# Kernel tuning notes

Measured on AMD Instinct MI355X. Metric: run time of the kernel, lower is better.

The kernel has to match this reference:

```python
import jax, jax.numpy as jnp
import numpy as np

D_MODEL = 768
N_HEAD = 12
D_HEAD = D_MODEL // N_HEAD
B, T = 2, 2048


def setup_inputs() -> dict:
    key = jax.random.key(0)
    k1, k2, k3 = jax.random.split(key, 3)
    x = jax.random.normal(k1, (B, T, D_MODEL), dtype=jnp.float32)
    w_attn = jax.random.normal(k2, (D_MODEL, 3 * D_MODEL), dtype=jnp.float32) * (1.0 / np.sqrt(D_MODEL))
    b_attn = jnp.zeros((3 * D_MODEL,), dtype=jnp.float32)
    w_proj = jax.random.normal(k3, (D_MODEL, D_MODEL), dtype=jnp.float32) * (1.0 / np.sqrt(D_MODEL))
    b_proj = jnp.zeros((D_MODEL,), dtype=jnp.float32)
    return {"x": x, "w_attn": w_attn, "b_attn": b_attn, "w_proj": w_proj, "b_proj": b_proj}


def reference(x, w_attn, b_attn, w_proj, b_proj):
    Bq, Tq, C = x.shape
    qkv = x @ w_attn + b_attn                                  # [B, T, 3C]
    qkv = qkv.reshape(Bq, Tq, 3, N_HEAD, D_HEAD)
    q, k, v = qkv[:, :, 0], qkv[:, :, 1], qkv[:, :, 2]         # [B, T, H, Dh]
    scale = 1.0 / np.sqrt(D_HEAD)
    att = jnp.einsum('bqhd,bkhd->bhqk', q, k) * scale          # [B, H, T, T]
    causal = jnp.tril(jnp.ones((Tq, Tq), dtype=bool))
    att = jnp.where(causal[None, None], att, -jnp.inf)
    att = jax.nn.softmax(att, axis=-1)
    y = jnp.einsum('bhqk,bkhd->bqhd', att, v).reshape(Bq, Tq, C)
    return y @ w_proj + b_proj
```

## Files before the change

kernel.cpp:

```cpp
#include <hip/hip_runtime.h>
#include <hip/hip_bf16.h>

#define D_MODEL 768
#define N_HEADS 12
#define D_HEADK 64
#define BB 2
#define TT 2048
#define M_TOK (BB*TT)
#define N_QKV (3*D_MODEL)
#define MS_SEG (BB*N_HEADS*TT)

using f32x4  = __attribute__((ext_vector_type(4))) float;
using f32x16 = __attribute__((ext_vector_type(16))) float;
using s16x8  = __attribute__((ext_vector_type(8))) short;

__device__ __forceinline__ float fast_exp2(float x) {
    return __builtin_amdgcn_exp2f(x);
}

__device__ __forceinline__ unsigned short f2bf(float f) {
    union { float f; unsigned u; } v; v.f = f;
    unsigned r = v.u + 0x7FFFu + ((v.u >> 16) & 1u);
    return (unsigned short)(r >> 16);
}

__device__ __forceinline__ float bf2f(unsigned short u) {
    union { unsigned u; float f; } v; v.u = ((unsigned)u) << 16; return v.f;
}

__device__ __forceinline__ unsigned cvtpk_bf16(float lo, float hi) {
    unsigned d;
    asm("v_cvt_pk_bf16_f32 %0, %1, %2" : "=v"(d) : "v"(lo), "v"(hi));
    return d;
}

__global__ void xbf_kernel(const float* __restrict__ X, unsigned short* __restrict__ Xb) {
    int idx = (blockIdx.x * 256 + threadIdx.x) * 8;
    float4 v0 = *(const float4*)&X[idx];
    float4 v1 = *(const float4*)&X[idx + 4];
    ushort4 u0, u1;
    u0.x = f2bf(v0.x); u0.y = f2bf(v0.y); u0.z = f2bf(v0.z); u0.w = f2bf(v0.w);
    u1.x = f2bf(v1.x); u1.y = f2bf(v1.y); u1.z = f2bf(v1.z); u1.w = f2bf(v1.w);
    *(ushort4*)&Xb[idx]     = u0;
    *(ushort4*)&Xb[idx + 4] = u1;
}

__global__ void wtrans_kernel(const float* __restrict__ Wa, const float* __restrict__ Wp,
                              unsigned short* __restrict__ Wta, unsigned short* __restrict__ Wtp) {
    const float* W; unsigned short* Wt; int N;
    if (blockIdx.z == 0) { W = Wa; Wt = Wta; N = N_QKV; }
    else                 { W = Wp; Wt = Wtp; N = D_MODEL; }
    int bx = blockIdx.x * 32;
    if (bx >= N) return;
    int by = blockIdx.y * 32;
    __shared__ float tile[32][33];
    int tx = threadIdx.x & 31;
    int ty = threadIdx.x >> 5;
    #pragma unroll
    for (int i = ty; i < 32; i += 8)
        tile[i][tx] = W[(size_t)(by + i) * N + bx + tx];
    __syncthreads();
    #pragma unroll
    for (int i = ty; i < 32; i += 8)
        Wt[(size_t)(bx + i) * D_MODEL + by + tx] = f2bf(tile[tx][i]);
}

__launch_bounds__(256)
__global__ void qkv_kernel(const unsigned short* __restrict__ Xb, const unsigned short* __restrict__ Wt,
                           const float* __restrict__ bias,
                           unsigned short* __restrict__ Qw, unsigned short* __restrict__ Kw,
                           unsigned short* __restrict__ Vw) {
    __shared__ unsigned short As[128][40];
    __shared__ unsigned short Bs[128][40];
    const int m0 = blockIdx.y * 128;
    const int n0 = blockIdx.x * 128;
    const int tid = threadIdx.x;
    const int l  = tid & 63;
    const int w  = tid >> 6;
    const int wr = w >> 1, wc = w & 1;
    const int lr = l & 15, lk = (l >> 4) * 8, li = (l >> 4) * 4;

    f32x4 acc[4][4] = {};
    for (int kt = 0; kt < D_MODEL; kt += 32) {
        #pragma unroll
        for (int p = 0; p < 2; ++p) {
            int ch = tid * 2 + p;
            int r = ch >> 2;
            int c = (ch & 3) * 8;
            *(int4*)&As[r][c] = *(const int4*)&Xb[(size_t)(m0 + r) * D_MODEL + kt + c];
            *(int4*)&Bs[r][c] = *(const int4*)&Wt[(size_t)(n0 + r) * D_MODEL + kt + c];
        }
        __syncthreads();
        s16x8 a[4], bf[4];
        #pragma unroll
        for (int mi = 0; mi < 4; ++mi)
            a[mi] = *(const s16x8*)&As[wr*64 + mi*16 + lr][lk];
        #pragma unroll
        for (int ni = 0; ni < 4; ++ni)
            bf[ni] = *(const s16x8*)&Bs[wc*64 + ni*16 + lr][lk];
        #pragma unroll
        for (int mi = 0; mi < 4; ++mi)
            #pragma unroll
            for (int ni = 0; ni < 4; ++ni)
                acc[mi][ni] = __builtin_amdgcn_mfma_f32_16x16x32_bf16(a[mi], bf[ni], acc[mi][ni], 0, 0, 0);
        __syncthreads();
    }
    #pragma unroll
    for (int ni = 0; ni < 4; ++ni) {
        int ng = n0 + wc*64 + ni*16 + lr;
        int mat = ng / D_MODEL;
        int hd  = ng % D_MODEL;
        int h = hd >> 6, d = hd & 63;
        float bv = bias[ng];
        #pragma unroll
        for (int mi = 0; mi < 4; ++mi) {
            #pragma unroll
            for (int i = 0; i < 4; ++i) {
                int t  = m0 + wr*64 + mi*16 + li + i;
                int b  = t >> 11, tq = t & 2047;
                float val = acc[mi][ni][i] + bv;
                size_t off = ((size_t)(b*N_HEADS + h)*TT + tq)*64 + d;
                if (mat == 0)      Qw[off] = f2bf(val * 0.18033688f);
                else if (mat == 1) Kw[off] = f2bf(val);
                else               Vw[off] = f2bf(val);
            }
        }
    }
}

__launch_bounds__(256)
__global__ void vtrans_kernel(const unsigned short* __restrict__ Vw, unsigned short* __restrict__ Vt) {
    __shared__ unsigned short tile[64][65];
    const int bh = blockIdx.y;
    const int t0 = blockIdx.x * 64;
    const int tid = threadIdx.x;
    const int srow = tid >> 3;
    const int scol = (tid & 7) * 8;
    const unsigned short* src = Vw + (size_t)bh * TT * 64;
    unsigned short* dst = Vt + (size_t)bh * 64 * TT;
    *(int4*)&tile[srow][scol]    = *(const int4*)&src[(size_t)(t0 + srow) * 64 + scol];
    *(int4*)&tile[srow+32][scol] = *(const int4*)&src[(size_t)(t0 + srow + 32) * 64 + scol];
    __syncthreads();
    s16x8 a0, a1;
    #pragma unroll
    for (int j = 0; j < 8; ++j) {
        a0[j] = (short)tile[scol + j][srow];
        a1[j] = (short)tile[scol + j][srow + 32];
    }
    *(s16x8*)&dst[(size_t)srow * TT + t0 + scol]        = a0;
    *(s16x8*)&dst[(size_t)(srow + 32) * TT + t0 + scol] = a1;
}

__device__ __forceinline__ int swz(int r, int c) { return r*64 + (c ^ ((r & 7) << 3)); }

__launch_bounds__(256)
__global__ void attn_kernel(const unsigned short* __restrict__ Q,
                            const unsigned short* __restrict__ Kk,
                            const unsigned short* __restrict__ Vt,
                            unsigned short* __restrict__ oA,
                            unsigned short* __restrict__ oB,
                            float* __restrict__ ms) {
    __shared__ unsigned short Ks[64*64];
    __shared__ unsigned short Vs[64*64];
    const int bh = blockIdx.y;
    const int px = blockIdx.x;
    const int qci = 15 - (px >> 1);
    const int seg = px & 1;
    const int q0 = qci * 128;
    const int b = bh / N_HEADS, h = bh % N_HEADS;
    const int tid = threadIdx.x;
    const int l  = tid & 63;
    const int w  = tid >> 6;
    const int lq = l & 31;
    const int hi = l >> 5;
    const int srow = tid >> 3;
    const int scol = (tid & 7) * 8;
    const int qw0 = q0 + w * 32;

    const unsigned short* Qp = Q  + (size_t)bh * TT * 64;
    const unsigned short* Kp = Kk + (size_t)bh * TT * 64;
    const unsigned short* Vp = Vt + (size_t)bh * 64 * TT;

    const int ntiles  = 2 * (qci + 1);
    const int n0      = ntiles >> 1;
    const int t_begin = seg ? n0 : 0;
    const int t_end   = seg ? ntiles : n0;

    s16x8 qsel[4];
    {
        const unsigned short* qrow = &Qp[(size_t)(qw0 + lq) * 64];
        #pragma unroll
        for (int t = 0; t < 4; ++t) {
            s16x8 qlo = *(const s16x8*)&qrow[16*t];
            s16x8 qhi = *(const s16x8*)&qrow[16*t + 8];
            qsel[t] = hi ? qhi : qlo;
        }
    }

    float mi = -1e30f, si = 0.f;
    f32x16 o0 = {}, o1 = {};

    const int kb0 = t_begin * 64;
    int4 kp0 = *(const int4*)&Kp[(size_t)(kb0 + srow) * 64 + scol];
    int4 kp1 = *(const int4*)&Kp[(size_t)(kb0 + srow + 32) * 64 + scol];
    int4 vp0 = *(const int4*)&Vp[(size_t)srow * TT + kb0 + scol];
    int4 vp1 = *(const int4*)&Vp[(size_t)(srow + 32) * TT + kb0 + scol];

    for (int it = t_begin; it < t_end; ++it) {
        const int kt = it * 64;
        __syncthreads();
        *(int4*)&Ks[swz(srow,      scol)] = kp0;
        *(int4*)&Ks[swz(srow + 32, scol)] = kp1;
        *(int4*)&Vs[swz(srow,      scol)] = vp0;
        *(int4*)&Vs[swz(srow + 32, scol)] = vp1;
        __syncthreads();
        if (it + 1 < t_end) {
            const int k2 = kt + 64;
            kp0 = *(const int4*)&Kp[(size_t)(k2 + srow) * 64 + scol];
            kp1 = *(const int4*)&Kp[(size_t)(k2 + srow + 32) * 64 + scol];
            vp0 = *(const int4*)&Vp[(size_t)srow * TT + k2 + scol];
            vp1 = *(const int4*)&Vp[(size_t)(srow + 32) * TT + k2 + scol];
        }
        #pragma unroll
        for (int kti = 0; kti < 2; ++kti) {
            const int kk = kt + kti * 32;
            if (kk > qw0) continue;
            const bool diag = (kk == qw0);
            f32x16 s = {};
            #pragma unroll
            for (int t = 0; t < 4; ++t) {
                s16x8 a = *(const s16x8*)&Ks[swz(kti*32 + lq, 16*t + 8*hi)];
                s = __builtin_amdgcn_mfma_f32_32x32x16_bf16(a, qsel[t], s, 0, 0, 0);
            }
            if (diag) {
                #pragma unroll
                for (int r = 0; r < 16; ++r) {
                    const int kloc = (r & 3) + 8*(r >> 2) + 4*hi;
                    if (kloc > lq) s[r] = -1e30f;
                }
            }
            float lm = s[0];
            #pragma unroll
            for (int r = 1; r < 16; ++r) lm = fmaxf(lm, s[r]);
            if (!__all(lm <= mi + 11.5f)) {
                float pm = fmaxf(lm, __shfl_xor(lm, 32));
                float mn = fmaxf(mi, pm);
                float sf = fast_exp2(mi - mn);
                si *= sf;
                #pragma unroll
                for (int r = 0; r < 16; ++r) {
                    const int qloc = (r & 3) + 8*(r >> 2) + 4*hi;
                    float sfq = __shfl(sf, qloc);
                    o0[r] *= sfq; o1[r] *= sfq;
                }
                mi = mn;
            }
            float e[16];
            float psum = 0.f;
            #pragma unroll
            for (int r = 0; r < 16; ++r) {
                e[r] = fast_exp2(s[r] - mi);
                psum += e[r];
            }
            si += psum;
            #pragma unroll
            for (int s2 = 0; s2 < 2; ++s2) {
                unsigned c0 = cvtpk_bf16(e[8*s2 + 0], e[8*s2 + 1]);
                unsigned c1 = cvtpk_bf16(e[8*s2 + 2], e[8*s2 + 3]);
                unsigned c2 = cvtpk_bf16(e[8*s2 + 4], e[8*s2 + 5]);
                unsigned c3 = cvtpk_bf16(e[8*s2 + 6], e[8*s2 + 7]);
                asm("v_permlane32_swap_b32 %0, %1" : "+v"(c0), "+v"(c2));
                asm("v_permlane32_swap_b32 %0, %1" : "+v"(c1), "+v"(c3));
                union { unsigned u[4]; s16x8 v; } pa;
                pa.u[0] = c0; pa.u[1] = c1; pa.u[2] = c2; pa.u[3] = c3;
                const int kc = kti*32 + 16*s2 + 8*hi;
                s16x8 vb0 = *(const s16x8*)&Vs[swz(lq,      kc)];
                s16x8 vb1 = *(const s16x8*)&Vs[swz(32 + lq, kc)];
                o0 = __builtin_amdgcn_mfma_f32_32x32x16_bf16(pa.v, vb0, o0, 0, 0, 0);
                o1 = __builtin_amdgcn_mfma_f32_32x32x16_bf16(pa.v, vb1, o1, 0, 0, 0);
            }
        }
    }
    float sfull = si + __shfl_xor(si, 32);
    if (hi == 0) {
        const int row = bh * TT + qw0 + lq;
        ms[seg*MS_SEG + row]            = mi;
        ms[2*MS_SEG + seg*MS_SEG + row] = sfull;
    }
    unsigned short* op = seg ? oB : oA;
    #pragma unroll
    for (int r = 0; r < 16; ++r) {
        const int qloc = (r & 3) + 8*(r >> 2) + 4*hi;
        size_t row = (size_t)(b*TT + qw0 + qloc) * D_MODEL + h*64;
        op[row + lq]      = f2bf(o0[r]);
        op[row + 32 + lq] = f2bf(o1[r]);
    }
}

__launch_bounds__(256)
__global__ void merge_kernel(const unsigned short* __restrict__ oA,
                             const unsigned short* __restrict__ oB,
                             const float* __restrict__ ms,
                             unsigned short* __restrict__ Yw) {
    const int gid = blockIdx.x * 256 + threadIdx.x;
    const int e = gid * 8;
    const int t = e / D_MODEL;
    const int c = e % D_MODEL;
    const int b = t >> 11, q = t & 2047;
    const int h = c >> 6;
    const int row = (b * N_HEADS + h) * TT + q;
    float m0 = ms[row],            m1 = ms[MS_SEG + row];
    float s0 = ms[2*MS_SEG + row], s1 = ms[3*MS_SEG + row];
    float m  = fmaxf(m0, m1);
    float a0 = fast_exp2(m0 - m), a1 = fast_exp2(m1 - m);
    float inv = 1.f / (s0 * a0 + s1 * a1);
    float w0 = a0 * inv, w1 = a1 * inv;
    s16x8 va = *(const s16x8*)&oA[e];
    s16x8 vb = *(const s16x8*)&oB[e];
    s16x8 out;
    #pragma unroll
    for (int j = 0; j < 8; ++j)
        out[j] = (short)f2bf(bf2f((unsigned short)va[j]) * w0 +
                             bf2f((unsigned short)vb[j]) * w1);
    *(s16x8*)&Yw[e] = out;
}

__launch_bounds__(256)
__global__ void proj_kernel(const unsigned short* __restrict__ Y, const unsigned short* __restrict__ Wt,
                            const float* __restrict__ bias, float* __restrict__ Out) {
    __shared__ unsigned short As[128][40];
    __shared__ unsigned short Bs[128][40];
    const int m0 = blockIdx.y * 128;
    const int n0 = blockIdx.x * 128;
    const int tid = threadIdx.x;
    const int l  = tid & 63;
    const int w  = tid >> 6;
    const int wr = w >> 1, wc = w & 1;
    const int lr = l & 15, lk = (l >> 4) * 8, li = (l >> 4) * 4;

    f32x4 acc[4][4] = {};
    for (int kt = 0; kt < D_MODEL; kt += 32) {
        #pragma unroll
        for (int p = 0; p < 2; ++p) {
            int ch = tid * 2 + p;
            int r = ch >> 2;
            int c = (ch & 3) * 8;
            *(int4*)&As[r][c] = *(const int4*)&Y[(size_t)(m0 + r) * D_MODEL + kt + c];
            *(int4*)&Bs[r][c] = *(const int4*)&Wt[(size_t)(n0 + r) * D_MODEL + kt + c];
        }
        __syncthreads();
        s16x8 a[4], bf[4];
        #pragma unroll
        for (int mi = 0; mi < 4; ++mi)
            a[mi] = *(const s16x8*)&As[wr*64 + mi*16 + lr][lk];
        #pragma unroll
        for (int ni = 0; ni < 4; ++ni)
            bf[ni] = *(const s16x8*)&Bs[wc*64 + ni*16 + lr][lk];
        #pragma unroll
        for (int mi = 0; mi < 4; ++mi)
            #pragma unroll
            for (int ni = 0; ni < 4; ++ni)
                acc[mi][ni] = __builtin_amdgcn_mfma_f32_16x16x32_bf16(a[mi], bf[ni], acc[mi][ni], 0, 0, 0);
        __syncthreads();
    }
    #pragma unroll
    for (int ni = 0; ni < 4; ++ni) {
        int ng = n0 + wc*64 + ni*16 + lr;
        float bv = bias[ng];
        #pragma unroll
        for (int mj = 0; mj < 4; ++mj)
            #pragma unroll
            for (int i = 0; i < 4; ++i) {
                int t = m0 + wr*64 + mj*16 + li + i;
                Out[(size_t)t*D_MODEL + ng] = acc[mj][ni][i] + bv;
            }
    }
}

extern "C" void kernel_launch(void* const* d_in, const int* in_sizes, int n_in,
                              void* d_out, int out_size, void* d_ws, size_t ws_size,
                              hipStream_t stream) {
    const float* x      = (const float*)d_in[0];
    const float* w_attn = (const float*)d_in[1];
    const float* b_attn = (const float*)d_in[2];
    const float* w_proj = (const float*)d_in[3];
    const float* b_proj = (const float*)d_in[4];
    float* out = (float*)d_out;

    unsigned short* wt_attn = (unsigned short*)d_ws;
    unsigned short* wt_proj = wt_attn + (size_t)N_QKV * D_MODEL;
    unsigned short* Qw      = wt_proj + (size_t)D_MODEL * D_MODEL;
    unsigned short* Kw      = Qw + (size_t)M_TOK * D_MODEL;
    unsigned short* Vw      = Kw + (size_t)M_TOK * D_MODEL;
    unsigned short* Yw      = Vw + (size_t)M_TOK * D_MODEL;
    unsigned short* Xb      = Yw + (size_t)M_TOK * D_MODEL;
    unsigned short* Vtw     = Xb;
    unsigned short* oA      = Vw;
    unsigned short* oB      = Yw;
    float*          msbuf   = (float*)d_ws;

    hipLaunchKernelGGL(xbf_kernel, dim3(M_TOK*D_MODEL/2048), dim3(256), 0, stream, x, Xb);
    hipLaunchKernelGGL(wtrans_kernel, dim3(N_QKV/32, D_MODEL/32, 2), dim3(256), 0, stream,
                       w_attn, w_proj, wt_attn, wt_proj);
    hipLaunchKernelGGL(qkv_kernel, dim3(N_QKV/128, M_TOK/128), dim3(256), 0, stream,
                       Xb, wt_attn, b_attn, Qw, Kw, Vw);
    hipLaunchKernelGGL(vtrans_kernel, dim3(TT/64, BB*N_HEADS), dim3(256), 0, stream,
                       Vw, Vtw);
    hipLaunchKernelGGL(attn_kernel, dim3(32, BB*N_HEADS), dim3(256), 0, stream,
                       Qw, Kw, Vtw, oA, oB, msbuf);
    hipLaunchKernelGGL(merge_kernel, dim3(M_TOK*D_MODEL/8/256), dim3(256), 0, stream,
                       oA, oB, msbuf, Yw);
    hipLaunchKernelGGL(proj_kernel, dim3(D_MODEL/128, M_TOK/128), dim3(256), 0, stream,
                       Yw, wt_proj, b_proj, out);
}
```

Baseline: 195.2 us.

## Split causal attention into four KV segments and stream QKV GEMM tiles into LDS

The attention kernel now splits each query block's KV range into four segments instead of two. This doubles the grid and should improve load balance across CUs, at the cost of two extra partial-output buffers and a four-way softmax-rescale merge. Separately, the QKV GEMM uses global_load_lds to copy 16-byte chunks straight into XOR-swizzled LDS, with a K-tile of 64. This removes the register round-trip on loads and halves the number of barriers. The risks are extra merge bandwidth and extra workspace for the oC and oD buffers.

```diff
diff --git a/kernel.cpp b/kernel.cpp
--- a/kernel.cpp
+++ b/kernel.cpp
@@ -13,6 +13,9 @@
 using f32x4  = __attribute__((ext_vector_type(4))) float;
 using f32x16 = __attribute__((ext_vector_type(16))) float;
 using s16x8  = __attribute__((ext_vector_type(8))) short;
+
+typedef __attribute__((address_space(1))) const unsigned int ga_u32;
+typedef __attribute__((address_space(3))) unsigned int ls_u32;
 
 __device__ __forceinline__ float fast_exp2(float x) {
     return __builtin_amdgcn_exp2f(x);
@@ -70,39 +73,53 @@
                            const float* __restrict__ bias,
                            unsigned short* __restrict__ Qw, unsigned short* __restrict__ Kw,
                            unsigned short* __restrict__ Vw) {
-    __shared__ unsigned short As[128][40];
-    __shared__ unsigned short Bs[128][40];
+    __shared__ unsigned short As[128*64];
+    __shared__ unsigned short Bs[128*64];
     const int m0 = blockIdx.y * 128;
     const int n0 = blockIdx.x * 128;
     const int tid = threadIdx.x;
     const int l  = tid & 63;
     const int w  = tid >> 6;
     const int wr = w >> 1, wc = w & 1;
-    const int lr = l & 15, lk = (l >> 4) * 8, li = (l >> 4) * 4;
+    const int lr = l & 15, lk4 = l >> 4, li = (l >> 4) * 4;
+    const int grw  = l >> 3;
+    const int gslt = l & 7;
 
     f32x4 acc[4][4] = {};
-    for (int kt = 0; kt < D_MODEL; kt += 32) {
-        #pragma unroll
-        for (int p = 0; p < 2; ++p) {
-            int ch = tid * 2 + p;
-            int r = ch >> 2;
-            int c = (ch & 3) * 8;
-            *(int4*)&As[r][c] = *(const int4*)&Xb[(size_t)(m0 + r) * D_MODEL + kt + c];
-            *(int4*)&Bs[r][c] = *(const int4*)&Wt[(size_t)(n0 + r) * D_MODEL + kt + c];
-        }
-        __syncthreads();
-        s16x8 a[4], bf[4];
-        #pragma unroll
-        for (int mi = 0; mi < 4; ++mi)
-            a[mi] = *(const s16x8*)&As[wr*64 + mi*16 + lr][lk];
-        #pragma unroll
-        for (int ni = 0; ni < 4; ++ni)
-            bf[ni] = *(const s16x8*)&Bs[wc*64 + ni*16 + lr][lk];
-        #pragma unroll
-        for (int mi = 0; mi < 4; ++mi)
-            #pragma unroll
-            for (int ni = 0; ni < 4; ++ni)
-                acc[mi][ni] = __builtin_amdgcn_mfma_f32_16x16x32_bf16(a[mi], bf[ni], acc[mi][ni], 0, 0, 0);
+    for (int kt = 0; kt < D_MODEL; kt += 64) {
+        #pragma unroll
+        for (int i = 0; i < 4; ++i) {
+            const int row  = w*32 + i*8 + grw;
+            const int gcol = (gslt ^ (row & 7)) << 3;
+            __builtin_amdgcn_global_load_lds(
+                (ga_u32*)&Xb[(size_t)(m0 + row) * D_MODEL + kt + gcol],
+                (ls_u32*)&As[(w*32 + i*8) * 64], 16, 0, 0);
+            __builtin_amdgcn_global_load_lds(
+                (ga_u32*)&Wt[(size_t)(n0 + row) * D_MODEL + kt + gcol],
+                (ls_u32*)&Bs[(w*32 + i*8) * 64], 16, 0, 0);
+        }
+        __syncthreads();
+        #pragma unroll
+        for (int ks = 0; ks < 2; ++ks) {
+            s16x8 a[4], bf[4];
+            #pragma unroll
+            for (int mi = 0; mi < 4; ++mi) {
+                const int row = wr*64 + mi*16 + lr;
+                const int slot = (ks*4 + lk4) ^ (row & 7);
+                a[mi] = *(const s16x8*)&As[row*64 + slot*8];
+            }
+            #pragma unroll
+            for (int ni = 0; ni < 4; ++ni) {
+                const int row = wc*64 + ni*16 + lr;
+                const int slot = (ks*4 + lk4) ^ (row & 7);
+                bf[ni] = *(const s16x8*)&Bs[row*64 + slot*8];
+            }
+            #pragma unroll
+            for (int mi = 0; mi < 4; ++mi)
+                #pragma unroll
+                for (int ni = 0; ni < 4; ++ni)
+                    acc[mi][ni] = __builtin_amdgcn_mfma_f32_16x16x32_bf16(a[mi], bf[ni], acc[mi][ni], 0, 0, 0);
+        }
         __syncthreads();
     }
     #pragma unroll
@@ -159,13 +176,15 @@
                             const unsigned short* __restrict__ Vt,
                             unsigned short* __restrict__ oA,
                             unsigned short* __restrict__ oB,
+                            unsigned short* __restrict__ oC,
+                            unsigned short* __restrict__ oD,
                             float* __restrict__ ms) {
     __shared__ unsigned short Ks[64*64];
     __shared__ unsigned short Vs[64*64];
     const int bh = blockIdx.y;
     const int px = blockIdx.x;
-    const int qci = 15 - (px >> 1);
-    const int seg = px & 1;
+    const int qci = 15 - (px >> 2);
+    const int seg = px & 3;
     const int q0 = qci * 128;
     const int b = bh / N_HEADS, h = bh % N_HEADS;
     const int tid = threadIdx.x;
@@ -182,9 +201,8 @@
     const unsigned short* Vp = Vt + (size_t)bh * 64 * TT;
 
     const int ntiles  = 2 * (qci + 1);
-    const int n0      = ntiles >> 1;
-    const int t_begin = seg ? n0 : 0;
-    const int t_end   = seg ? ntiles : n0;
+    const int t_begin = (seg * ntiles) >> 2;
+    const int t_end   = ((seg + 1) * ntiles) >> 2;
 
     s16x8 qsel[4];
     {
@@ -284,10 +302,10 @@
     float sfull = si + __shfl_xor(si, 32);
     if (hi == 0) {
         const int row = bh * TT + qw0 + lq;
-        ms[seg*MS_SEG + row]            = mi;
-        ms[2*MS_SEG + seg*MS_SEG + row] = sfull;
-    }
-    unsigned short* op = seg ? oB : oA;
+        ms[seg*MS_SEG + row]       = mi;
+        ms[(4+seg)*MS_SEG + row]   = sfull;
+    }
+    unsigned short* op = (seg == 0) ? oA : (seg == 1) ? oB : (seg == 2) ? oC : oD;
     #pragma unroll
     for (int r = 0; r < 16; ++r) {
         const int qloc = (r & 3) + 8*(r >> 2) + 4*hi;
@@ -300,6 +318,8 @@
 __launch_bounds__(256)
 __global__ void merge_kernel(const unsigned short* __restrict__ oA,
                              const unsigned short* __restrict__ oB,
+                             const unsigned short* __restrict__ oC,
+                             const unsigned short* __restrict__ oD,
                              const float* __restrict__ ms,
                              unsigned short* __restrict__ Yw) {
     const int gid = blockIdx.x * 256 + threadIdx.x;
@@ -310,18 +330,25 @@
     const int h = c >> 6;
     const int row = (b * N_HEADS + h) * TT + q;
     float m0 = ms[row],            m1 = ms[MS_SEG + row];
-    float s0 = ms[2*MS_SEG + row], s1 = ms[3*MS_SEG + row];
-    float m  = fmaxf(m0, m1);
+    float m2 = ms[2*MS_SEG + row], m3 = ms[3*MS_SEG + row];
+    float s0 = ms[4*MS_SEG + row], s1 = ms[5*MS_SEG + row];
+    float s2 = ms[6*MS_SEG + row], s3 = ms[7*MS_SEG + row];
+    float m  = fmaxf(fmaxf(m0, m1), fmaxf(m2, m3));
     float a0 = fast_exp2(m0 - m), a1 = fast_exp2(m1 - m);
-    float inv = 1.f / (s0 * a0 + s1 * a1);
-    float w0 = a0 * inv, w1 = a1 * inv;
+    float a2 = fast_exp2(m2 - m), a3 = fast_exp2(m3 - m);
+    float inv = 1.f / (s0*a0 + s1*a1 + s2*a2 + s3*a3);
+    float w0 = a0*inv, w1 = a1*inv, w2 = a2*inv, w3 = a3*inv;
     s16x8 va = *(const s16x8*)&oA[e];
     s16x8 vb = *(const s16x8*)&oB[e];
+    s16x8 vc = *(const s16x8*)&oC[e];
+    s16x8 vd = *(const s16x8*)&oD[e];
     s16x8 out;
     #pragma unroll
     for (int j = 0; j < 8; ++j)
         out[j] = (short)f2bf(bf2f((unsigned short)va[j]) * w0 +
-                             bf2f((unsigned short)vb[j]) * w1);
+                             bf2f((unsigned short)vb[j]) * w1 +
+                             bf2f((unsigned short)vc[j]) * w2 +
+                             bf2f((unsigned short)vd[j]) * w3);
     *(s16x8*)&Yw[e] = out;
 }
 
@@ -394,6 +421,8 @@
     unsigned short* Vw      = Kw + (size_t)M_TOK * D_MODEL;
     unsigned short* Yw      = Vw + (size_t)M_TOK * D_MODEL;
     unsigned short* Xb      = Yw + (size_t)M_TOK * D_MODEL;
+    unsigned short* oC      = Xb + (size_t)M_TOK * D_MODEL;
+    unsigned short* oD      = oC + (size_t)M_TOK * D_MODEL;
     unsigned short* Vtw     = Xb;
     unsigned short* oA      = Vw;
     unsigned short* oB      = Yw;
@@ -406,10 +435,10 @@
                        Xb, wt_attn, b_attn, Qw, Kw, Vw);
     hipLaunchKernelGGL(vtrans_kernel, dim3(TT/64, BB*N_HEADS), dim3(256), 0, stream,
                        Vw, Vtw);
-    hipLaunchKernelGGL(attn_kernel, dim3(32, BB*N_HEADS), dim3(256), 0, stream,
-                       Qw, Kw, Vtw, oA, oB, msbuf);
+    hipLaunchKernelGGL(attn_kernel, dim3(64, BB*N_HEADS), dim3(256), 0, stream,
+                       Qw, Kw, Vtw, oA, oB, oC, oD, msbuf);
     hipLaunchKernelGGL(merge_kernel, dim3(M_TOK*D_MODEL/8/256), dim3(256), 0, stream,
-                       oA, oB, msbuf, Yw);
+                       oA, oB, oC, oD, msbuf, Yw);
     hipLaunchKernelGGL(proj_kernel, dim3(D_MODEL/128, M_TOK/128), dim3(256), 0, stream,
                        Yw, wt_proj, b_proj, out);
 }
```

New measurement: 196.7 us. About the same (+0.8%).
